# Kernel tuning notes

Measured on AMD Instinct MI355X. Metric: run time of the kernel, lower is better.

Reference implementation:

```python
import jax, jax.numpy as jnp
import numpy as np

NEG_SLOPE = 0.2  # LeakyReLU(0.2) on the final Dense


def setup_inputs() -> dict:
    key = jax.random.key(0)
    k1, k2, k3, k4 = jax.random.split(key, 4)
    B, D = 256, 65536          # batch, input voxel dim
    N, G = 41, 2048            # n_groups, group size (overlapping allowed)
    O, E = 256, 512            # per-group output dim, embed_dim
    x = jax.random.normal(k1, (B, D), dtype=jnp.float32)
    group_idx = jax.random.randint(k2, (N, G), 0, D, dtype=jnp.int32)
    # He-normal-ish init for the per-group Dense weights
    W = jax.random.normal(k3, (N, G, O), dtype=jnp.float32) * np.float32(np.sqrt(2.0 / G))
    b = jnp.zeros((N, O), dtype=jnp.float32)
    W3 = jax.random.normal(k4, (N * O, E), dtype=jnp.float32) * np.float32(np.sqrt(2.0 / (N * O)))
    b3 = jnp.zeros((E,), dtype=jnp.float32)
    return {"x": x, "group_idx": group_idx, "W": W, "b": b, "W3": W3, "b3": b3}


def reference(x, group_idx, W, b, W3, b3):
    B = x.shape[0]
    # per-group gather: (B, N, G)
    g = x[:, group_idx]
    # N parallel Dense layers as one grouped GEMM: (B, N, O)
    h = jnp.einsum('bng,ngo->bno', g, W) + b
    # concat along feature axis -> (B, N*O); dropout is identity at inference
    h = h.reshape(B, -1)
    # final Dense + LeakyReLU(0.2)
    out = h @ W3 + b3
    return jnp.where(out >= 0, out, NEG_SLOPE * out)
```

## Files before the change

kernel.cpp:

```cpp
#include <hip/hip_runtime.h>
#include <hip/hip_bf16.h>

#define NB 256
#define DD 65536
#define NN 41
#define GG 2048
#define OO 256
#define NO 10496
#define EE 512
#define NEG_SLOPE 0.2f

typedef __attribute__((ext_vector_type(8))) short bf16x8;
typedef __attribute__((ext_vector_type(4))) float f32x4;
typedef unsigned int u32;

__global__ __launch_bounds__(256) void transpose_cast_k(const float* __restrict__ src,
                                                        __hip_bfloat16* __restrict__ dst,
                                                        int K, int Oc) {
    __shared__ float tile[32][33];
    size_t slab = (size_t)blockIdx.z * K * Oc;
    int k0 = blockIdx.y * 32, o0 = blockIdx.x * 32;
    int tx = threadIdx.x & 31, ty = threadIdx.x >> 5;
    const float* s = src + slab;
#pragma unroll
    for (int i = 0; i < 4; ++i)
        tile[ty + 8 * i][tx] = s[(size_t)(k0 + ty + 8 * i) * Oc + o0 + tx];
    __syncthreads();
    __hip_bfloat16* d = dst + slab;
    int o = threadIdx.x >> 4;
    int kp = threadIdx.x & 15;
#pragma unroll
    for (int i2 = 0; i2 < 2; ++i2) {
        int oo = o + 16 * i2;
        __hip_bfloat162 p;
        p.x = __float2bfloat16(tile[2 * kp][oo]);
        p.y = __float2bfloat16(tile[2 * kp + 1][oo]);
        *(__hip_bfloat162*)&d[(size_t)(o0 + oo) * K + k0 + 2 * kp] = p;
    }
}

__global__ __launch_bounds__(512) void gather_half_k(const float* __restrict__ x,
                                                     const int* __restrict__ idx,
                                                     __hip_bfloat16* __restrict__ g) {
    __shared__ __align__(16) __hip_bfloat16 xr[32768];
    int b = blockIdx.x >> 1;
    int h = blockIdx.x & 1;
    int t = threadIdx.x;
    const float4* xv = (const float4*)(x + (size_t)b * DD + h * 32768);
#pragma unroll
    for (int i = 0; i < 16; ++i) {
        float4 v = xv[t + 512 * i];
        short4 p;
        p.x = (short)__bfloat16_as_ushort(__float2bfloat16(v.x));
        p.y = (short)__bfloat16_as_ushort(__float2bfloat16(v.y));
        p.z = (short)__bfloat16_as_ushort(__float2bfloat16(v.z));
        p.w = (short)__bfloat16_as_ushort(__float2bfloat16(v.w));
        *(short4*)&xr[(t + 512 * i) * 4] = p;
    }
    __syncthreads();
    const int4* idx4 = (const int4*)idx;
    for (int u = t; u < NN * GG / 4; u += 512) {
        int4 ii = idx4[u];
        int n = u >> 9;
        int k = (u & 511) * 4;
        __hip_bfloat16* dst = &g[((size_t)n * NB + b) * GG + k];
        if ((ii.x >> 15) == h) dst[0] = xr[ii.x & 32767];
        if ((ii.y >> 15) == h) dst[1] = xr[ii.y & 32767];
        if ((ii.z >> 15) == h) dst[2] = xr[ii.z & 32767];
        if ((ii.w >> 15) == h) dst[3] = xr[ii.w & 32767];
    }
}

__global__ __launch_bounds__(512) void gemm1_k(const __hip_bfloat16* __restrict__ g,
                                               const __hip_bfloat16* __restrict__ Wt,
                                               float* __restrict__ part1) {
    int bid = blockIdx.x;
    int n = bid >> 3;
    int s = bid & 1;
    int m0 = ((bid >> 1) & 1) * 128;
    int o0 = ((bid >> 2) & 1) * 128;
    const u32* srcA = (const u32*)(g + ((size_t)n * NB + m0) * GG);
    const u32* srcB = (const u32*)(Wt + ((size_t)n * OO + o0) * GG);
    __shared__ __align__(16) __hip_bfloat16 lA[128 * 32];
    __shared__ __align__(16) __hip_bfloat16 lB[128 * 32];
    int t = threadIdx.x;
    int lane = t & 63, w = t >> 6;
    int mw = (w >> 2) * 64;
    int nw = (w & 3) * 32;
    int lrow = lane & 15, quad = lane >> 4;
    f32x4 acc[4][2] = {};

    for (int k0 = s * 1024; k0 < s * 1024 + 1024; k0 += 32) {
        __syncthreads();
        int kw = k0 >> 1;
#pragma unroll
        for (int i = 0; i < 4; ++i) {
            int u = t + 512 * i;
            int r = u >> 4, kk = u & 15;
            ((u32*)lA)[r * 16 + kk] = srcA[(size_t)r * (GG / 2) + kw + kk];
        }
#pragma unroll
        for (int i = 0; i < 4; ++i) {
            int u = t + 512 * i;
            int r = u >> 4, kk = u & 15;
            ((u32*)lB)[r * 16 + kk] = srcB[(size_t)r * (GG / 2) + kw + kk];
        }
        __syncthreads();
        bf16x8 af[4];
#pragma unroll
        for (int fm = 0; fm < 4; ++fm)
            af[fm] = *(const bf16x8*)&lA[(mw + fm * 16 + lrow) * 32 + quad * 8];
#pragma unroll
        for (int fn = 0; fn < 2; ++fn) {
            bf16x8 bfr = *(const bf16x8*)&lB[(nw + fn * 16 + lrow) * 32 + quad * 8];
#pragma unroll
            for (int fm = 0; fm < 4; ++fm)
                acc[fm][fn] = __builtin_amdgcn_mfma_f32_16x16x32_bf16(af[fm], bfr, acc[fm][fn], 0, 0, 0);
        }
    }
#pragma unroll
    for (int fm = 0; fm < 4; ++fm) {
#pragma unroll
        for (int fn = 0; fn < 2; ++fn) {
            int col = o0 + nw + fn * 16 + lrow;
#pragma unroll
            for (int r = 0; r < 4; ++r) {
                int row = m0 + mw + fm * 16 + quad * 4 + r;
                part1[((size_t)s * NB + row) * NO + n * OO + col] = acc[fm][fn][r];
            }
        }
    }
}

__global__ __launch_bounds__(256) void combine1_k(const float* __restrict__ part1,
                                                  const float* __restrict__ bias,
                                                  __hip_bfloat16* __restrict__ h) {
    int j4 = blockIdx.x * 256 + threadIdx.x;
    const float4* p0 = (const float4*)part1;
    const float4* p1 = p0 + (size_t)NB * NO / 4;
    int jj = j4 % (NO / 4);
    float4 a = p0[j4], c = p1[j4];
    float4 bv = ((const float4*)bias)[jj];
    a.x += c.x + bv.x; a.y += c.y + bv.y; a.z += c.z + bv.z; a.w += c.w + bv.w;
    ushort4 o;
    o.x = __bfloat16_as_ushort(__float2bfloat16(a.x));
    o.y = __bfloat16_as_ushort(__float2bfloat16(a.y));
    o.z = __bfloat16_as_ushort(__float2bfloat16(a.z));
    o.w = __bfloat16_as_ushort(__float2bfloat16(a.w));
    *(ushort4*)&h[(size_t)j4 * 4] = o;
}

__global__ __launch_bounds__(256) void gemm2_k(const __hip_bfloat16* __restrict__ h,
                                               const __hip_bfloat16* __restrict__ W3t,
                                               float* __restrict__ part) {
    int bid = blockIdx.x;
    int s = bid >> 4;
    int m0 = ((bid >> 3) & 1) * 128;
    int e0 = (bid & 7) * 64;
    const u32* srcA = (const u32*)h + (size_t)m0 * (NO / 2);
    const u32* srcB = (const u32*)(W3t + (size_t)e0 * NO);
    __shared__ __align__(16) __hip_bfloat16 lA[128 * 32];
    __shared__ __align__(16) __hip_bfloat16 lB[64 * 32];
    int t = threadIdx.x;
    int lane = t & 63, w = t >> 6;
    int mw = (w >> 1) * 64, nw = (w & 1) * 32;
    int lrow = lane & 15, quad = lane >> 4;
    f32x4 acc[4][2] = {};

    for (int k0 = s * 256; k0 < s * 256 + 256; k0 += 32) {
        __syncthreads();
        int kw = k0 >> 1;
#pragma unroll
        for (int i = 0; i < 8; ++i) {
            int u = t + 256 * i;
            int r = u >> 4, kk = u & 15;
            ((u32*)lA)[r * 16 + kk] = srcA[(size_t)r * (NO / 2) + kw + kk];
        }
#pragma unroll
        for (int i = 0; i < 4; ++i) {
            int u = t + 256 * i;
            int r = u >> 4, kk = u & 15;
            ((u32*)lB)[r * 16 + kk] = srcB[(size_t)r * (NO / 2) + kw + kk];
        }
        __syncthreads();
        bf16x8 af[4];
#pragma unroll
        for (int fm = 0; fm < 4; ++fm)
            af[fm] = *(const bf16x8*)&lA[(mw + fm * 16 + lrow) * 32 + quad * 8];
#pragma unroll
        for (int fn = 0; fn < 2; ++fn) {
            bf16x8 bfr = *(const bf16x8*)&lB[(nw + fn * 16 + lrow) * 32 + quad * 8];
#pragma unroll
            for (int fm = 0; fm < 4; ++fm)
                acc[fm][fn] = __builtin_amdgcn_mfma_f32_16x16x32_bf16(af[fm], bfr, acc[fm][fn], 0, 0, 0);
        }
    }
#pragma unroll
    for (int fm = 0; fm < 4; ++fm) {
#pragma unroll
        for (int fn = 0; fn < 2; ++fn) {
            int e = e0 + nw + fn * 16 + lrow;
#pragma unroll
            for (int r = 0; r < 4; ++r) {
                int row = m0 + mw + fm * 16 + quad * 4 + r;
                part[((size_t)s * NB + row) * EE + e] = acc[fm][fn][r];
            }
        }
    }
}

__global__ __launch_bounds__(256) void reduce_k(const float* __restrict__ part,
                                                const float* __restrict__ b3,
                                                float* __restrict__ out) {
    int j = blockIdx.x * 256 + threadIdx.x;
    float4 a = make_float4(0.f, 0.f, 0.f, 0.f);
    for (int s = 0; s < NN; ++s) {
        float4 v = ((const float4*)part)[(size_t)s * (NB * EE / 4) + j];
        a.x += v.x; a.y += v.y; a.z += v.z; a.w += v.w;
    }
    float4 bv = ((const float4*)b3)[j & 127];
    a.x += bv.x; a.y += bv.y; a.z += bv.z; a.w += bv.w;
    a.x = a.x >= 0.f ? a.x : NEG_SLOPE * a.x;
    a.y = a.y >= 0.f ? a.y : NEG_SLOPE * a.y;
    a.z = a.z >= 0.f ? a.z : NEG_SLOPE * a.z;
    a.w = a.w >= 0.f ? a.w : NEG_SLOPE * a.w;
    ((float4*)out)[j] = a;
}

extern "C" void kernel_launch(void* const* d_in, const int* in_sizes, int n_in,
                              void* d_out, int out_size, void* d_ws, size_t ws_size,
                              hipStream_t stream) {
    const float* x = (const float*)d_in[0];
    const int* idx = (const int*)d_in[1];
    const float* W = (const float*)d_in[2];
    const float* bias = (const float*)d_in[3];
    const float* W3 = (const float*)d_in[4];
    const float* b3 = (const float*)d_in[5];
    float* out = (float*)d_out;

    char* ws = (char*)d_ws;
    const size_t g_off = 0;
    const size_t g_sz = (size_t)NN * NB * GG * 2;
    const size_t wt_off = g_off + g_sz;
    const size_t wt_sz = (size_t)NN * GG * OO * 2;
    const size_t w3t_off = wt_off + wt_sz;
    const size_t w3t_sz = (size_t)NO * EE * 2;
    const size_t h_off = w3t_off + w3t_sz;
    const size_t h_sz = (size_t)NB * NO * 2;
    const size_t p_off = h_off + h_sz;

    __hip_bfloat16* g = (__hip_bfloat16*)(ws + g_off);
    __hip_bfloat16* Wt = (__hip_bfloat16*)(ws + wt_off);
    __hip_bfloat16* W3t = (__hip_bfloat16*)(ws + w3t_off);
    __hip_bfloat16* h = (__hip_bfloat16*)(ws + h_off);
    float* part1 = (float*)(ws + p_off);
    float* part = (float*)(ws + p_off);

    transpose_cast_k<<<dim3(OO / 32, GG / 32, NN), 256, 0, stream>>>(W, Wt, GG, OO);
    transpose_cast_k<<<dim3(EE / 32, NO / 32, 1), 256, 0, stream>>>(W3, W3t, NO, EE);
    gather_half_k<<<dim3(512), 512, 0, stream>>>(x, idx, g);
    gemm1_k<<<dim3(328), 512, 0, stream>>>(g, Wt, part1);
    combine1_k<<<dim3(NB * NO / 4 / 256), 256, 0, stream>>>(part1, bias, h);
    gemm2_k<<<dim3(656), 256, 0, stream>>>(h, W3t, part);
    reduce_k<<<dim3(128), 256, 0, stream>>>(part, b3, out);
}
```

Measured before the change: 313.2 us.

## Fuse bias into GEMM1, use direct global-to-LDS loads, full-row gather

The split-K partials in GEMM1 are removed, and the bias add and bf16 cast are fused into its epilogue, so the combine kernel and its fp32 round trip go away. Both GEMMs now use global_load_lds 16-byte direct loads with larger 128x128 tiles per 256-thread block. The gather kernel stages a whole x row in 128KB of dynamic LDS and writes vectorised ushort4 outputs, avoiding the two-pass half-row filtering. The trade-off is fewer blocks (164 and 328 on a large GPU), which means lower occupancy and less parallelism, and the gather needs the large-LDS attribute to be accepted.

```diff
diff --git a/kernel.cpp b/kernel.cpp
--- a/kernel.cpp
+++ b/kernel.cpp
@@ -14,6 +14,11 @@
 typedef __attribute__((ext_vector_type(4))) float f32x4;
 typedef unsigned int u32;
 
+__device__ __forceinline__ void gl_lds16(const __hip_bfloat16* gsrc, __hip_bfloat16* lds) {
+    __builtin_amdgcn_global_load_lds((const __attribute__((address_space(1))) u32*)gsrc,
+                                     (__attribute__((address_space(3))) u32*)lds, 16, 0, 0);
+}
+
 __global__ __launch_bounds__(256) void transpose_cast_k(const float* __restrict__ src,
                                                         __hip_bfloat16* __restrict__ dst,
                                                         int K, int Oc) {
@@ -36,6 +41,40 @@
         p.x = __float2bfloat16(tile[2 * kp][oo]);
         p.y = __float2bfloat16(tile[2 * kp + 1][oo]);
         *(__hip_bfloat162*)&d[(size_t)(o0 + oo) * K + k0 + 2 * kp] = p;
+    }
+}
+
+__global__ __launch_bounds__(512) void gather_full_k(const float* __restrict__ x,
+                                                     const int* __restrict__ idx,
+                                                     __hip_bfloat16* __restrict__ g) {
+    extern __shared__ __hip_bfloat16 xr[];
+    int b = blockIdx.x;
+    int t = threadIdx.x;
+    const float4* xv = (const float4*)(x + (size_t)b * DD);
+#pragma unroll
+    for (int i = 0; i < 32; ++i) {
+        float4 v = xv[t + 512 * i];
+        short4 p;
+        p.x = (short)__bfloat16_as_ushort(__float2bfloat16(v.x));
+        p.y = (short)__bfloat16_as_ushort(__float2bfloat16(v.y));
+        p.z = (short)__bfloat16_as_ushort(__float2bfloat16(v.z));
+        p.w = (short)__bfloat16_as_ushort(__float2bfloat16(v.w));
+        *(short4*)&xr[(t + 512 * i) * 4] = p;
+    }
+    __syncthreads();
+    const int4* idx4 = (const int4*)idx;
+#pragma unroll 1
+    for (int it = 0; it < 41; ++it) {
+        int u = t + 512 * it;
+        int n = u >> 9;
+        int k = (u & 511) * 4;
+        int4 ii = idx4[u];
+        ushort4 o;
+        o.x = __bfloat16_as_ushort(xr[ii.x]);
+        o.y = __bfloat16_as_ushort(xr[ii.y]);
+        o.z = __bfloat16_as_ushort(xr[ii.z]);
+        o.w = __bfloat16_as_ushort(xr[ii.w]);
+        *(ushort4*)&g[((size_t)n * NB + b) * GG + k] = o;
     }
 }
 
@@ -71,47 +110,38 @@
     }
 }
 
-__global__ __launch_bounds__(512) void gemm1_k(const __hip_bfloat16* __restrict__ g,
+__global__ __launch_bounds__(256) void gemm1_k(const __hip_bfloat16* __restrict__ g,
                                                const __hip_bfloat16* __restrict__ Wt,
-                                               float* __restrict__ part1) {
+                                               const float* __restrict__ bias,
+                                               __hip_bfloat16* __restrict__ h) {
     int bid = blockIdx.x;
-    int n = bid >> 3;
-    int s = bid & 1;
+    int n = bid >> 2;
     int m0 = ((bid >> 1) & 1) * 128;
-    int o0 = ((bid >> 2) & 1) * 128;
-    const u32* srcA = (const u32*)(g + ((size_t)n * NB + m0) * GG);
-    const u32* srcB = (const u32*)(Wt + ((size_t)n * OO + o0) * GG);
+    int o0 = (bid & 1) * 128;
+    const __hip_bfloat16* srcA = g + ((size_t)n * NB + m0) * GG;
+    const __hip_bfloat16* srcB = Wt + ((size_t)n * OO + o0) * GG;
     __shared__ __align__(16) __hip_bfloat16 lA[128 * 32];
     __shared__ __align__(16) __hip_bfloat16 lB[128 * 32];
     int t = threadIdx.x;
     int lane = t & 63, w = t >> 6;
-    int mw = (w >> 2) * 64;
-    int nw = (w & 3) * 32;
+    int mw = (w >> 1) * 64, nw = (w & 1) * 64;
     int lrow = lane & 15, quad = lane >> 4;
-    f32x4 acc[4][2] = {};
-
-    for (int k0 = s * 1024; k0 < s * 1024 + 1024; k0 += 32) {
-        __syncthreads();
-        int kw = k0 >> 1;
-#pragma unroll
-        for (int i = 0; i < 4; ++i) {
-            int u = t + 512 * i;
-            int r = u >> 4, kk = u & 15;
-            ((u32*)lA)[r * 16 + kk] = srcA[(size_t)r * (GG / 2) + kw + kk];
-        }
-#pragma unroll
-        for (int i = 0; i < 4; ++i) {
-            int u = t + 512 * i;
-            int r = u >> 4, kk = u & 15;
-            ((u32*)lB)[r * 16 + kk] = srcB[(size_t)r * (GG / 2) + kw + kk];
-        }
+    int r0 = t >> 2, q0 = (t & 3) * 8;
+    f32x4 acc[4][4] = {};
+
+    for (int k0 = 0; k0 < GG; k0 += 32) {
+        __syncthreads();
+        gl_lds16(srcA + (size_t)r0 * GG + k0 + q0, lA + t * 8);
+        gl_lds16(srcA + (size_t)(r0 + 64) * GG + k0 + q0, lA + (t + 256) * 8);
+        gl_lds16(srcB + (size_t)r0 * GG + k0 + q0, lB + t * 8);
+        gl_lds16(srcB + (size_t)(r0 + 64) * GG + k0 + q0, lB + (t + 256) * 8);
         __syncthreads();
         bf16x8 af[4];
 #pragma unroll
         for (int fm = 0; fm < 4; ++fm)
             af[fm] = *(const bf16x8*)&lA[(mw + fm * 16 + lrow) * 32 + quad * 8];
 #pragma unroll
-        for (int fn = 0; fn < 2; ++fn) {
+        for (int fn = 0; fn < 4; ++fn) {
             bf16x8 bfr = *(const bf16x8*)&lB[(nw + fn * 16 + lrow) * 32 + quad * 8];
 #pragma unroll
             for (int fm = 0; fm < 4; ++fm)
@@ -121,74 +151,49 @@
 #pragma unroll
     for (int fm = 0; fm < 4; ++fm) {
 #pragma unroll
-        for (int fn = 0; fn < 2; ++fn) {
+        for (int fn = 0; fn < 4; ++fn) {
             int col = o0 + nw + fn * 16 + lrow;
+            float bv = bias[n * OO + col];
 #pragma unroll
             for (int r = 0; r < 4; ++r) {
                 int row = m0 + mw + fm * 16 + quad * 4 + r;
-                part1[((size_t)s * NB + row) * NO + n * OO + col] = acc[fm][fn][r];
+                h[(size_t)row * NO + n * OO + col] = __float2bfloat16(acc[fm][fn][r] + bv);
             }
         }
     }
-}
-
-__global__ __launch_bounds__(256) void combine1_k(const float* __restrict__ part1,
-                                                  const float* __restrict__ bias,
-                                                  __hip_bfloat16* __restrict__ h) {
-    int j4 = blockIdx.x * 256 + threadIdx.x;
-    const float4* p0 = (const float4*)part1;
-    const float4* p1 = p0 + (size_t)NB * NO / 4;
-    int jj = j4 % (NO / 4);
-    float4 a = p0[j4], c = p1[j4];
-    float4 bv = ((const float4*)bias)[jj];
-    a.x += c.x + bv.x; a.y += c.y + bv.y; a.z += c.z + bv.z; a.w += c.w + bv.w;
-    ushort4 o;
-    o.x = __bfloat16_as_ushort(__float2bfloat16(a.x));
-    o.y = __bfloat16_as_ushort(__float2bfloat16(a.y));
-    o.z = __bfloat16_as_ushort(__float2bfloat16(a.z));
-    o.w = __bfloat16_as_ushort(__float2bfloat16(a.w));
-    *(ushort4*)&h[(size_t)j4 * 4] = o;
 }
 
 __global__ __launch_bounds__(256) void gemm2_k(const __hip_bfloat16* __restrict__ h,
                                                const __hip_bfloat16* __restrict__ W3t,
                                                float* __restrict__ part) {
     int bid = blockIdx.x;
-    int s = bid >> 4;
-    int m0 = ((bid >> 3) & 1) * 128;
-    int e0 = (bid & 7) * 64;
-    const u32* srcA = (const u32*)h + (size_t)m0 * (NO / 2);
-    const u32* srcB = (const u32*)(W3t + (size_t)e0 * NO);
+    int s = bid >> 3;
+    int m0 = ((bid >> 2) & 1) * 128;
+    int e0 = (bid & 3) * 128;
+    const __hip_bfloat16* srcA = h + (size_t)m0 * NO;
+    const __hip_bfloat16* srcB = W3t + (size_t)e0 * NO;
     __shared__ __align__(16) __hip_bfloat16 lA[128 * 32];
-    __shared__ __align__(16) __hip_bfloat16 lB[64 * 32];
+    __shared__ __align__(16) __hip_bfloat16 lB[128 * 32];
     int t = threadIdx.x;
     int lane = t & 63, w = t >> 6;
-    int mw = (w >> 1) * 64, nw = (w & 1) * 32;
+    int mw = (w >> 1) * 64, nw = (w & 1) * 64;
     int lrow = lane & 15, quad = lane >> 4;
-    f32x4 acc[4][2] = {};
+    int r0 = t >> 2, q0 = (t & 3) * 8;
+    f32x4 acc[4][4] = {};
 
     for (int k0 = s * 256; k0 < s * 256 + 256; k0 += 32) {
         __syncthreads();
-        int kw = k0 >> 1;
-#pragma unroll
-        for (int i = 0; i < 8; ++i) {
-            int u = t + 256 * i;
-            int r = u >> 4, kk = u & 15;
-            ((u32*)lA)[r * 16 + kk] = srcA[(size_t)r * (NO / 2) + kw + kk];
-        }
-#pragma unroll
-        for (int i = 0; i < 4; ++i) {
-            int u = t + 256 * i;
-            int r = u >> 4, kk = u & 15;
-            ((u32*)lB)[r * 16 + kk] = srcB[(size_t)r * (NO / 2) + kw + kk];
-        }
+        gl_lds16(srcA + (size_t)r0 * NO + k0 + q0, lA + t * 8);
+        gl_lds16(srcA + (size_t)(r0 + 64) * NO + k0 + q0, lA + (t + 256) * 8);
+        gl_lds16(srcB + (size_t)r0 * NO + k0 + q0, lB + t * 8);
+        gl_lds16(srcB + (size_t)(r0 + 64) * NO + k0 + q0, lB + (t + 256) * 8);
         __syncthreads();
         bf16x8 af[4];
 #pragma unroll
         for (int fm = 0; fm < 4; ++fm)
             af[fm] = *(const bf16x8*)&lA[(mw + fm * 16 + lrow) * 32 + quad * 8];
 #pragma unroll
-        for (int fn = 0; fn < 2; ++fn) {
+        for (int fn = 0; fn < 4; ++fn) {
             bf16x8 bfr = *(const bf16x8*)&lB[(nw + fn * 16 + lrow) * 32 + quad * 8];
 #pragma unroll
             for (int fm = 0; fm < 4; ++fm)
@@ -198,7 +203,7 @@
 #pragma unroll
     for (int fm = 0; fm < 4; ++fm) {
 #pragma unroll
-        for (int fn = 0; fn < 2; ++fn) {
+        for (int fn = 0; fn < 4; ++fn) {
             int e = e0 + nw + fn * 16 + lrow;
 #pragma unroll
             for (int r = 0; r < 4; ++r) {
@@ -253,14 +258,18 @@
     __hip_bfloat16* Wt = (__hip_bfloat16*)(ws + wt_off);
     __hip_bfloat16* W3t = (__hip_bfloat16*)(ws + w3t_off);
     __hip_bfloat16* h = (__hip_bfloat16*)(ws + h_off);
-    float* part1 = (float*)(ws + p_off);
     float* part = (float*)(ws + p_off);
 
     transpose_cast_k<<<dim3(OO / 32, GG / 32, NN), 256, 0, stream>>>(W, Wt, GG, OO);
     transpose_cast_k<<<dim3(EE / 32, NO / 32, 1), 256, 0, stream>>>(W3, W3t, NO, EE);
-    gather_half_k<<<dim3(512), 512, 0, stream>>>(x, idx, g);
-    gemm1_k<<<dim3(328), 512, 0, stream>>>(g, Wt, part1);
-    combine1_k<<<dim3(NB * NO / 4 / 256), 256, 0, stream>>>(part1, bias, h);
-    gemm2_k<<<dim3(656), 256, 0, stream>>>(h, W3t, part);
+    hipError_t aerr = hipFuncSetAttribute(reinterpret_cast<const void*>(gather_full_k),
+                                          hipFuncAttributeMaxDynamicSharedMemorySize, 131072);
+    if (aerr == hipSuccess) {
+        gather_full_k<<<dim3(NB), 512, 131072, stream>>>(x, idx, g);
+    } else {
+        gather_half_k<<<dim3(512), 512, 0, stream>>>(x, idx, g);
+    }
+    gemm1_k<<<dim3(164), 256, 0, stream>>>(g, Wt, bias, h);
+    gemm2_k<<<dim3(328), 256, 0, stream>>>(h, W3t, part);
     reduce_k<<<dim3(128), 256, 0, stream>>>(part, b3, out);
 }
```

Measured after the change: 308.5 us. About the same (-1.5%).
